# Kernel optimization log

Measured on AMD Instinct MI355X. Metric: run time of the kernel, lower is better.

## Reference

```python
import jax, jax.numpy as jnp
import numpy as np

NUM_CLASSES = 19
RMI_RADIUS = 3
POOL_SIZE = 3
POOL_STRIDE = 3
IGNORE_INDEX = 255
LOSS_WEIGHT = 1.0


def _avg_pool_nchw(x, k, s):
    # torch F.avg_pool2d with padding=k//2, count_include_pad=True
    p = k // 2
    summed = jax.lax.reduce_window(
        x, 0.0, jax.lax.add,
        window_dimensions=(1, 1, k, k),
        window_strides=(1, 1, s, s),
        padding=[(0, 0), (0, 0), (p, p), (p, p)])
    return summed / float(k * k)


def _map_get_pairs(labels, probs, radius):
    h, w = labels.shape[2], labels.shape[3]
    nh, nw = h - radius + 1, w - radius + 1
    la = jnp.stack([labels[:, :, y:y + nh, x:x + nw]
                    for y in range(radius) for x in range(radius)], axis=2)
    pr = jnp.stack([probs[:, :, y:y + nh, x:x + nw]
                    for y in range(radius) for x in range(radius)], axis=2)
    return la, pr  # (N, C, r*r, nh, nw)


def _log_det_by_cholesky(mat):
    chol = jnp.linalg.cholesky(mat)
    diag = jnp.diagonal(chol, axis1=-2, axis2=-1)
    return 2.0 * jnp.sum(jnp.log(diag + 1e-8), axis=-1)


def _rmi_lower_bound(labels_4d, probs_4d):
    labels_4d = _avg_pool_nchw(labels_4d, POOL_SIZE, POOL_STRIDE)
    probs_4d = _avg_pool_nchw(probs_4d, POOL_SIZE, POOL_STRIDE)
    la, pr = _map_get_pairs(labels_4d, probs_4d, RMI_RADIUS)
    N, C, D = la.shape[:3]
    la = la.reshape(N, C, D, -1)   # (N, C, D, M)
    pr = pr.reshape(N, C, D, -1)
    M = la.shape[-1]
    la = la - la.mean(axis=-1, keepdims=True)
    pr = pr - pr.mean(axis=-1, keepdims=True)
    la_cov = jnp.einsum('ncdm,ncem->ncde', la, la) / M
    pr_cov = jnp.einsum('ncdm,ncem->ncde', pr, pr) / M
    pr_la_cov = jnp.einsum('ncdm,ncem->ncde', pr, la) / M
    eye = jnp.eye(D, dtype=la_cov.dtype)
    la_cov_inv = jnp.linalg.inv(la_cov + eye * 1e-5)
    appro_var = pr_cov - jnp.einsum('ncde,ncef,ncgf->ncdg',
                                    pr_la_cov, la_cov_inv, pr_la_cov)
    appro_var = appro_var + eye * 1e-6
    rmi_per_class = 0.5 * _log_det_by_cholesky(appro_var)  # (N, C)
    rmi_per_class = rmi_per_class.mean(axis=0)             # (C,)
    return jnp.sum(rmi_per_class) / NUM_CLASSES


def setup_inputs() -> dict:
    key = jax.random.key(0)
    k1, k2 = jax.random.split(key)
    cls_score = jax.random.normal(k1, (4, 19, 512, 512), dtype=jnp.float32)
    label = jax.random.randint(k2, (4, 512, 512), 0, NUM_CLASSES, dtype=jnp.int64)
    return {"cls_score": cls_score, "label": label}


def reference(cls_score, label):
    probs = jax.nn.softmax(cls_score.astype(jnp.float32), axis=1)
    valid = (label >= 0) & (label < NUM_CLASSES) & (label != IGNORE_INDEX)
    lbl = jnp.where(valid, label, 0)
    onehot = jax.nn.one_hot(lbl, NUM_CLASSES, dtype=jnp.float32)
    onehot = jnp.transpose(onehot, (0, 3, 1, 2))  # (N, C, H, W)
    vmask = valid[:, None, :, :].astype(jnp.float32)
    onehot = onehot * vmask
    probs = probs * vmask
    loss = _rmi_lower_bound(onehot, probs)
    return LOSS_WEIGHT * loss
```

## Files before the change

### kernel.cpp

```cpp
#include <hip/hip_runtime.h>
#include <math.h>

#define NBATCH 4
#define NCLS   19
#define HWDIM  512
#define HW     (512 * 512)
#define PH     171
#define PHP    176
#define PP2A   (171 * 176)
#define NHW    169
#define MM     (169 * 169)

typedef float f4  __attribute__((ext_vector_type(4)));
typedef float f2v __attribute__((ext_vector_type(2)));

__global__ __launch_bounds__(512) void stage1_pool(
    const float* __restrict__ cls, const int* __restrict__ label,
    float* __restrict__ P, float* __restrict__ L) {
  int n  = blockIdx.x / PH;
  int ph = blockIdx.x - n * PH;
  int col = threadIdx.x;

  float vv[3][NCLS];
  int lbs[3];
#pragma unroll
  for (int i = 0; i < 3; ++i) {
    int r = 3 * ph - 1 + i;
    bool ok = (r >= 0) && (r < HWDIM);
    if (ok) {
      lbs[i] = label[((size_t)n * HWDIM + r) * HWDIM + col];
      const float* base = cls + (size_t)n * NCLS * HW + (size_t)r * HWDIM + col;
#pragma unroll
      for (int c = 0; c < NCLS; ++c) vv[i][c] = base[(size_t)c * HW];
    } else {
      lbs[i] = -1;
#pragma unroll
      for (int c = 0; c < NCLS; ++c) vv[i][c] = 0.f;
    }
  }

  float accP[NCLS], accL[NCLS];
#pragma unroll
  for (int c = 0; c < NCLS; ++c) { accP[c] = 0.f; accL[c] = 0.f; }
#pragma unroll
  for (int i = 0; i < 3; ++i) {
    int lb = lbs[i];
    float mx = vv[i][0];
#pragma unroll
    for (int c = 1; c < NCLS; ++c) mx = fmaxf(mx, vv[i][c]);
    float se = 0.f;
    float ex[NCLS];
#pragma unroll
    for (int c = 0; c < NCLS; ++c) {
      ex[c] = __expf(vv[i][c] - mx);
      se += ex[c];
    }
    float m = (lb >= 0 && lb < NCLS) ? 1.f : 0.f;
    float inv = m / se;
#pragma unroll
    for (int c = 0; c < NCLS; ++c) {
      accP[c] += ex[c] * inv;
      accL[c] += (lb == c) ? 1.f : 0.f;
    }
  }

  __shared__ float xbP[10][516];
  __shared__ float xbL[10][516];
  const float inv9 = 1.f / 9.f;
#pragma unroll
  for (int c0 = 0; c0 < NCLS; c0 += 10) {
#pragma unroll
    for (int cc = 0; cc < 10; ++cc) {
      if (c0 + cc < NCLS) {
        xbP[cc][1 + col] = accP[(c0 + cc) < NCLS ? (c0 + cc) : 0];
        xbL[cc][1 + col] = accL[(c0 + cc) < NCLS ? (c0 + cc) : 0];
        if (col == 0) { xbP[cc][0] = 0.f; xbL[cc][0] = 0.f; }
      }
    }
    __syncthreads();
    if (col < PH) {
      int pw = col;
#pragma unroll
      for (int cc = 0; cc < 10; ++cc) {
        if (c0 + cc < NCLS) {
          int c = c0 + cc;
          float sP = xbP[cc][3 * pw] + xbP[cc][3 * pw + 1] + xbP[cc][3 * pw + 2];
          float sL = xbL[cc][3 * pw] + xbL[cc][3 * pw + 1] + xbL[cc][3 * pw + 2];
          size_t o = ((size_t)(n * NCLS + c)) * PP2A + (size_t)ph * PHP + pw;
          P[o] = sP * inv9;
          L[o] = sL * inv9;
        }
      }
    } else if (col < PHP) {
#pragma unroll
      for (int cc = 0; cc < 10; ++cc) {
        if (c0 + cc < NCLS) {
          int c = c0 + cc;
          size_t o = ((size_t)(n * NCLS + c)) * PP2A + (size_t)ph * PHP + col;
          P[o] = 0.f;
          L[o] = 0.f;
        }
      }
    }
    __syncthreads();
  }
}

template <int MODE, int NA>
__device__ __forceinline__ void epilogue(const f2v (&acc2)[NA], float* red,
                                         float* __restrict__ covp, int nc) {
  int lane = threadIdx.x & 63;
  int wid  = threadIdx.x >> 6;
#pragma unroll
  for (int k = 0; k < NA; ++k) {
    float v = acc2[k].x + acc2[k].y;
    v += __shfl_down(v, 32, 64);
    v += __shfl_down(v, 16, 64);
    v += __shfl_down(v, 8, 64);
    if (lane < 8) red[(wid * 8 + lane) * 84 + k] = v;
  }
  __syncthreads();
  int tid = threadIdx.x;
  if (tid < NA) {
    float sm = 0.f;
#pragma unroll
    for (int w = 0; w < 64; ++w) sm += red[w * 84 + tid];
    int off;
    if (MODE == 0)      off = (tid < 9) ? tid : 18 + (tid - 9);
    else if (MODE == 1) off = (tid < 9) ? 9 + tid : 63 + (tid - 9);
    else                off = 108 + tid;
    covp[(size_t)nc * 192 + off] = sm;
  }
}

__device__ __forceinline__ void fma_self_triple(f2v (&acc2)[54],
    const f2v (&r0)[5], const f2v (&r1)[5], const f2v (&r2)[5]) {
#define RP(d, off) ((d) < 3 ? r0[(d) % 3 + (off)] \
                 : (d) < 6 ? r1[(d) % 3 + (off)] : r2[(d) % 3 + (off)])
#pragma unroll
  for (int d = 0; d < 9; ++d) {
    acc2[d] += RP(d, 0);
    acc2[d] += RP(d, 2);
  }
  {
    int k = 9;
#pragma unroll
    for (int d = 0; d < 9; ++d)
#pragma unroll
      for (int e = d; e < 9; ++e) {
        acc2[k] += RP(d, 0) * RP(e, 0);
        acc2[k] += RP(d, 2) * RP(e, 2);
        ++k;
      }
  }
#undef RP
}

__device__ __forceinline__ void fma_cross_triple(f2v (&acc2)[81],
    const f2v (&p0)[3], const f2v (&p1)[3], const f2v (&p2)[3],
    const f2v (&l0)[3], const f2v (&l1)[3], const f2v (&l2)[3]) {
#define QP(d) ((d) < 3 ? p0[(d) % 3] : (d) < 6 ? p1[(d) % 3] : p2[(d) % 3])
#define QL(e) ((e) < 3 ? l0[(e) % 3] : (e) < 6 ? l1[(e) % 3] : l2[(e) % 3])
#pragma unroll
  for (int d = 0; d < 9; ++d)
#pragma unroll
    for (int e = 0; e < 9; ++e)
      acc2[d * 9 + e] += QP(d) * QL(e);
#undef QP
#undef QL
}

template <int MODE>
__device__ __forceinline__ void mom_self(const float* __restrict__ X,
                                         float* __restrict__ covp, int nc,
                                         float* red) {
  f2v acc2[54];
#pragma unroll
  for (int k = 0; k < 54; ++k) acc2[k] = (f2v){0.f, 0.f};

  int tid = threadIdx.x;
  if (tid < 462) {
    int b = tid / 42, s = tid - b * 42;
    int x0 = 4 * s;
    int y0 = (NHW * b) / 11;
    int y1 = (NHW * (b + 1)) / 11;

    f2v s0[5], s1[5], s2[5], s3[5];
    auto ldr = [&](f2v (&dst)[5], int row) {
      if (row > PH - 1) row = PH - 1;
      f4  a  = *(const f4*)(X + row * PHP + x0);
      f2v bb = *(const f2v*)(X + row * PHP + x0 + 4);
      dst[0] = (f2v){a.x, a.y}; dst[1] = (f2v){a.y, a.z};
      dst[2] = (f2v){a.z, a.w}; dst[3] = (f2v){a.w, bb.x};
      dst[4] = bb;
    };
    ldr(s0, y0); ldr(s1, y0 + 1); ldr(s2, y0 + 2);

    int y = y0;
    int span = y1 - y0;
    int nf = span & ~3;
    for (int i = 0; i < nf; i += 4, y += 4) {
      ldr(s3, y + 3); fma_self_triple(acc2, s0, s1, s2);
      ldr(s0, y + 4); fma_self_triple(acc2, s1, s2, s3);
      ldr(s1, y + 5); fma_self_triple(acc2, s2, s3, s0);
      ldr(s2, y + 6); fma_self_triple(acc2, s3, s0, s1);
    }
    int r = span & 3;
    if (r > 0) { ldr(s3, y + 3); fma_self_triple(acc2, s0, s1, s2); ++y; }
    if (r > 1) { ldr(s0, y + 3); fma_self_triple(acc2, s1, s2, s3); ++y; }
    if (r > 2) { ldr(s1, y + 3); fma_self_triple(acc2, s2, s3, s0); ++y; }
  } else if (tid < 473) {
    int b  = tid - 462;
    int y0 = (NHW * b) / 11;
    int y1 = (NHW * (b + 1)) / 11;
    float t[3][3];
#pragma unroll
    for (int r = 0; r < 3; ++r)
#pragma unroll
      for (int c = 0; c < 3; ++c) t[r][c] = X[(y0 + r) * PHP + 168 + c];
    for (int y = y0; y < y1; ++y) {
      int yn = (y + 3 <= PH - 1) ? (y + 3) : (PH - 1);
      float n0 = X[yn * PHP + 168], n1 = X[yn * PHP + 169],
            n2 = X[yn * PHP + 170];
#pragma unroll
      for (int d = 0; d < 9; ++d) acc2[d].x += t[d / 3][d % 3];
      {
        int k = 9;
#pragma unroll
        for (int d = 0; d < 9; ++d)
#pragma unroll
          for (int e = d; e < 9; ++e) {
            acc2[k].x += t[d / 3][d % 3] * t[e / 3][e % 3];
            ++k;
          }
      }
#pragma unroll
      for (int c = 0; c < 3; ++c) { t[0][c] = t[1][c]; t[1][c] = t[2][c]; }
      t[2][0] = n0; t[2][1] = n1; t[2][2] = n2;
    }
  }
  epilogue<MODE, 54>(acc2, red, covp, nc);
}

__device__ __forceinline__ void mom_cross(const float* __restrict__ Pp,
                                          const float* __restrict__ Lp,
                                          float* __restrict__ covp, int nc,
                                          float* red) {
  f2v acc2[81];
#pragma unroll
  for (int k = 0; k < 81; ++k) acc2[k] = (f2v){0.f, 0.f};

  int tid = threadIdx.x;
  if (tid < 504) {
    int b = tid / 84, s = tid - b * 84;
    int x0 = 2 * s;
    int y0 = (NHW * b) / 6;
    int y1 = (NHW * (b + 1)) / 6;

    f2v p0[3], p1[3], p2[3], p3[3];
    f2v l0[3], l1[3], l2[3], l3[3];
    auto ldc = [&](f2v (&dp)[3], f2v (&dl)[3], int row) {
      if (row > PH - 1) row = PH - 1;
      f2v a = *(const f2v*)(Pp + row * PHP + x0);
      f2v bb = *(const f2v*)(Pp + row * PHP + x0 + 2);
      dp[0] = a; dp[1] = (f2v){a.y, bb.x}; dp[2] = bb;
      f2v c = *(const f2v*)(Lp + row * PHP + x0);
      f2v d = *(const f2v*)(Lp + row * PHP + x0 + 2);
      dl[0] = c; dl[1] = (f2v){c.y, d.x}; dl[2] = d;
    };
    ldc(p0, l0, y0); ldc(p1, l1, y0 + 1); ldc(p2, l2, y0 + 2);

    int y = y0;
    int span = y1 - y0;
    int nf = span & ~3;
    for (int i = 0; i < nf; i += 4, y += 4) {
      ldc(p3, l3, y + 3); fma_cross_triple(acc2, p0, p1, p2, l0, l1, l2);
      ldc(p0, l0, y + 4); fma_cross_triple(acc2, p1, p2, p3, l1, l2, l3);
      ldc(p1, l1, y + 5); fma_cross_triple(acc2, p2, p3, p0, l2, l3, l0);
      ldc(p2, l2, y + 6); fma_cross_triple(acc2, p3, p0, p1, l3, l0, l1);
    }
    int r = span & 3;
    if (r > 0) { ldc(p3, l3, y + 3); fma_cross_triple(acc2, p0, p1, p2, l0, l1, l2); ++y; }
    if (r > 1) { ldc(p0, l0, y + 3); fma_cross_triple(acc2, p1, p2, p3, l1, l2, l3); ++y; }
    if (r > 2) { ldc(p1, l1, y + 3); fma_cross_triple(acc2, p2, p3, p0, l2, l3, l0); ++y; }
  } else if (tid < 510) {
    int b  = tid - 504;
    int y0 = (NHW * b) / 6;
    int y1 = (NHW * (b + 1)) / 6;
    float tp[3][3], tl[3][3];
#pragma unroll
    for (int r = 0; r < 3; ++r)
#pragma unroll
      for (int c = 0; c < 3; ++c) {
        tp[r][c] = Pp[(y0 + r) * PHP + 168 + c];
        tl[r][c] = Lp[(y0 + r) * PHP + 168 + c];
      }
    for (int y = y0; y < y1; ++y) {
      int yn = (y + 3 <= PH - 1) ? (y + 3) : (PH - 1);
      float np0 = Pp[yn * PHP + 168], np1 = Pp[yn * PHP + 169],
            np2 = Pp[yn * PHP + 170];
      float nl0 = Lp[yn * PHP + 168], nl1 = Lp[yn * PHP + 169],
            nl2 = Lp[yn * PHP + 170];
#pragma unroll
      for (int d = 0; d < 9; ++d)
#pragma unroll
        for (int e = 0; e < 9; ++e)
          acc2[d * 9 + e].x += tp[d / 3][d % 3] * tl[e / 3][e % 3];
#pragma unroll
      for (int c = 0; c < 3; ++c) {
        tp[0][c] = tp[1][c]; tp[1][c] = tp[2][c];
        tl[0][c] = tl[1][c]; tl[1][c] = tl[2][c];
      }
      tp[2][0] = np0; tp[2][1] = np1; tp[2][2] = np2;
      tl[2][0] = nl0; tl[2][1] = nl1; tl[2][2] = nl2;
    }
  }
  epilogue<2, 81>(acc2, red, covp, nc);
}

__global__ __launch_bounds__(512) void stage2_mom(
    const float* __restrict__ P, const float* __restrict__ L,
    float* __restrict__ covp) {
  __shared__ float red[64 * 84];
  int nc = blockIdx.x;
  const float* Pp = P + (size_t)nc * PP2A;
  const float* Lp = L + (size_t)nc * PP2A;
  if (blockIdx.y == 0)      mom_self<0>(Lp, covp, nc, red);
  else if (blockIdx.y == 1) mom_self<1>(Pp, covp, nc, red);
  else                      mom_cross(Pp, Lp, covp, nc, red);
}

__global__ __launch_bounds__(64) void stage3_rmi(float* __restrict__ covp) {
  int nc  = blockIdx.x;
  int tid = threadIdx.x;
  const float* s = covp + (size_t)nc * 192;
  __shared__ double lc[81], pc[81], plc[81], mla[9], mpr[9];
  const double Minv = 1.0 / (double)MM;

  if (tid < 9)       mla[tid]     = (double)s[tid] * Minv;
  else if (tid < 18) mpr[tid - 9] = (double)s[tid] * Minv;
  __syncthreads();

  for (int e = tid; e < 81; e += 64) {
    int r = e / 9, c = e - 9 * (e / 9);
    int lo = r < c ? r : c, hi = r < c ? c : r;
    int k = lo * 9 - lo * (lo - 1) / 2 + (hi - lo);
    double a = (double)s[18 + k] * Minv - mla[r] * mla[c];
    if (r == c) a += 1e-5;
    lc[e] = a;
    pc[e] = (double)s[63 + k] * Minv - mpr[r] * mpr[c];
    plc[e] = (double)s[108 + e] * Minv - mpr[r] * mla[c];
  }
  __syncthreads();

  for (int j = 0; j < 9; ++j) {
    if (tid == 0) lc[j * 9 + j] = sqrt(lc[j * 9 + j]);
    __syncthreads();
    if (tid > j && tid < 9) lc[tid * 9 + j] /= lc[j * 9 + j];
    __syncthreads();
    if (tid > j && tid < 9) {
      double lij = lc[tid * 9 + j];
      for (int k = j + 1; k <= tid; ++k) lc[tid * 9 + k] -= lij * lc[k * 9 + j];
    }
    __syncthreads();
  }

  if (tid < 9) {
    int d = tid;
    for (int j = 0; j < 9; ++j) {
      double t = plc[d * 9 + j];
      for (int k = 0; k < j; ++k) t -= plc[d * 9 + k] * lc[j * 9 + k];
      plc[d * 9 + j] = t / lc[j * 9 + j];
    }
  }
  __syncthreads();

  for (int e = tid; e < 81; e += 64) {
    int r = e / 9, c = e - 9 * (e / 9);
    double a = pc[e];
    for (int f = 0; f < 9; ++f) a -= plc[r * 9 + f] * plc[c * 9 + f];
    if (r == c) a += 1e-6;
    pc[e] = a;
  }
  __syncthreads();

  for (int j = 0; j < 9; ++j) {
    if (tid == 0) pc[j * 9 + j] = sqrt(pc[j * 9 + j]);
    __syncthreads();
    if (tid > j && tid < 9) pc[tid * 9 + j] /= pc[j * 9 + j];
    __syncthreads();
    if (tid > j && tid < 9) {
      double lij = pc[tid * 9 + j];
      for (int k = j + 1; k <= tid; ++k) pc[tid * 9 + k] -= lij * pc[k * 9 + j];
    }
    __syncthreads();
  }

  if (tid == 0) {
    double sl = 0.0;
    for (int j = 0; j < 9; ++j) sl += log(pc[j * 9 + j] + 1e-8);
    *(double*)(covp + (size_t)nc * 192 + 190) = sl;
  }
}

__global__ __launch_bounds__(64) void stage4_reduce(
    const float* __restrict__ covp, float* __restrict__ out) {
  int tid = threadIdx.x;
  double v = 0.0;
  if (tid < NBATCH * NCLS)
    v = *(const double*)(covp + (size_t)tid * 192 + 190);
  if (tid + 64 < NBATCH * NCLS)
    v += *(const double*)(covp + (size_t)(tid + 64) * 192 + 190);
#pragma unroll
  for (int o = 32; o > 0; o >>= 1) v += __shfl_down(v, o, 64);
  if (tid == 0) out[0] = (float)(v / (double)(NBATCH * NCLS));
}

extern "C" void kernel_launch(void* const* d_in, const int* in_sizes, int n_in,
                              void* d_out, int out_size, void* d_ws, size_t ws_size,
                              hipStream_t stream) {
  const float* cls  = (const float*)d_in[0];
  const int* label  = (const int*)d_in[1];
  float* out = (float*)d_out;

  float* P    = (float*)d_ws;
  float* L    = P + (size_t)NBATCH * NCLS * PP2A;
  float* covp = L + (size_t)NBATCH * NCLS * PP2A;

  stage1_pool<<<NBATCH * PH, 512, 0, stream>>>(cls, label, P, L);
  dim3 g2(NBATCH * NCLS, 3, 1);
  stage2_mom<<<g2, 512, 0, stream>>>(P, L, covp);
  stage3_rmi<<<NBATCH * NCLS, 64, 0, stream>>>(covp);
  stage4_reduce<<<1, 64, 0, stream>>>(covp, out);
}
```

Baseline: 72.49 us.

## Split cross-covariance moment block into three row-offset blocks

The 81-entry cross-covariance accumulation is split across three separate blocks, one per probability row offset G, so each block holds 27 accumulators instead of 81. This lowers register pressure in the heaviest block and raises the stage-2 grid from 3 to 5 blocks per (n,c), evening out the load across blocks. In exchange, the label rows are reloaded in each of the three blocks and the launch has more blocks.

```diff
diff --git a/kernel.cpp b/kernel.cpp
--- a/kernel.cpp
+++ b/kernel.cpp
@@ -128,7 +128,7 @@
     int off;
     if (MODE == 0)      off = (tid < 9) ? tid : 18 + (tid - 9);
     else if (MODE == 1) off = (tid < 9) ? 9 + tid : 63 + (tid - 9);
-    else                off = 108 + tid;
+    else                off = 108 + 27 * (MODE - 2) + tid;
     covp[(size_t)nc * 192 + off] = sm;
   }
 }
@@ -156,17 +156,15 @@
 #undef RP
 }
 
-__device__ __forceinline__ void fma_cross_triple(f2v (&acc2)[81],
-    const f2v (&p0)[3], const f2v (&p1)[3], const f2v (&p2)[3],
+__device__ __forceinline__ void fma_cross_g(f2v (&acc2)[27],
+    const f2v (&q)[3],
     const f2v (&l0)[3], const f2v (&l1)[3], const f2v (&l2)[3]) {
-#define QP(d) ((d) < 3 ? p0[(d) % 3] : (d) < 6 ? p1[(d) % 3] : p2[(d) % 3])
 #define QL(e) ((e) < 3 ? l0[(e) % 3] : (e) < 6 ? l1[(e) % 3] : l2[(e) % 3])
 #pragma unroll
-  for (int d = 0; d < 9; ++d)
+  for (int dx = 0; dx < 3; ++dx)
 #pragma unroll
     for (int e = 0; e < 9; ++e)
-      acc2[d * 9 + e] += QP(d) * QL(e);
-#undef QP
+      acc2[dx * 9 + e] += q[dx] * QL(e);
 #undef QL
 }
 
@@ -242,13 +240,14 @@
   epilogue<MODE, 54>(acc2, red, covp, nc);
 }
 
-__device__ __forceinline__ void mom_cross(const float* __restrict__ Pp,
-                                          const float* __restrict__ Lp,
-                                          float* __restrict__ covp, int nc,
-                                          float* red) {
-  f2v acc2[81];
-#pragma unroll
-  for (int k = 0; k < 81; ++k) acc2[k] = (f2v){0.f, 0.f};
+template <int G>
+__device__ __forceinline__ void mom_cross_g(const float* __restrict__ Pp,
+                                            const float* __restrict__ Lp,
+                                            float* __restrict__ covp, int nc,
+                                            float* red) {
+  f2v acc2[27];
+#pragma unroll
+  for (int k = 0; k < 27; ++k) acc2[k] = (f2v){0.f, 0.f};
 
   int tid = threadIdx.x;
   if (tid < 504) {
@@ -257,65 +256,58 @@
     int y0 = (NHW * b) / 6;
     int y1 = (NHW * (b + 1)) / 6;
 
-    f2v p0[3], p1[3], p2[3], p3[3];
     f2v l0[3], l1[3], l2[3], l3[3];
-    auto ldc = [&](f2v (&dp)[3], f2v (&dl)[3], int row) {
+    f2v q0[3], q1[3];
+    auto ldl = [&](f2v (&d)[3], int row) {
       if (row > PH - 1) row = PH - 1;
-      f2v a = *(const f2v*)(Pp + row * PHP + x0);
+      f2v a  = *(const f2v*)(Lp + row * PHP + x0);
+      f2v bb = *(const f2v*)(Lp + row * PHP + x0 + 2);
+      d[0] = a; d[1] = (f2v){a.y, bb.x}; d[2] = bb;
+    };
+    auto ldq = [&](f2v (&d)[3], int row) {
+      if (row > PH - 1) row = PH - 1;
+      f2v a  = *(const f2v*)(Pp + row * PHP + x0);
       f2v bb = *(const f2v*)(Pp + row * PHP + x0 + 2);
-      dp[0] = a; dp[1] = (f2v){a.y, bb.x}; dp[2] = bb;
-      f2v c = *(const f2v*)(Lp + row * PHP + x0);
-      f2v d = *(const f2v*)(Lp + row * PHP + x0 + 2);
-      dl[0] = c; dl[1] = (f2v){c.y, d.x}; dl[2] = d;
+      d[0] = a; d[1] = (f2v){a.y, bb.x}; d[2] = bb;
     };
-    ldc(p0, l0, y0); ldc(p1, l1, y0 + 1); ldc(p2, l2, y0 + 2);
+    ldl(l0, y0); ldl(l1, y0 + 1); ldl(l2, y0 + 2); ldq(q0, y0 + G);
 
     int y = y0;
     int span = y1 - y0;
     int nf = span & ~3;
     for (int i = 0; i < nf; i += 4, y += 4) {
-      ldc(p3, l3, y + 3); fma_cross_triple(acc2, p0, p1, p2, l0, l1, l2);
-      ldc(p0, l0, y + 4); fma_cross_triple(acc2, p1, p2, p3, l1, l2, l3);
-      ldc(p1, l1, y + 5); fma_cross_triple(acc2, p2, p3, p0, l2, l3, l0);
-      ldc(p2, l2, y + 6); fma_cross_triple(acc2, p3, p0, p1, l3, l0, l1);
+      ldl(l3, y + 3); ldq(q1, y + G + 1); fma_cross_g(acc2, q0, l0, l1, l2);
+      ldl(l0, y + 4); ldq(q0, y + G + 2); fma_cross_g(acc2, q1, l1, l2, l3);
+      ldl(l1, y + 5); ldq(q1, y + G + 3); fma_cross_g(acc2, q0, l2, l3, l0);
+      ldl(l2, y + 6); ldq(q0, y + G + 4); fma_cross_g(acc2, q1, l3, l0, l1);
     }
     int r = span & 3;
-    if (r > 0) { ldc(p3, l3, y + 3); fma_cross_triple(acc2, p0, p1, p2, l0, l1, l2); ++y; }
-    if (r > 1) { ldc(p0, l0, y + 3); fma_cross_triple(acc2, p1, p2, p3, l1, l2, l3); ++y; }
-    if (r > 2) { ldc(p1, l1, y + 3); fma_cross_triple(acc2, p2, p3, p0, l2, l3, l0); ++y; }
+    if (r > 0) { ldl(l3, y + 3); ldq(q1, y + G + 1);
+                 fma_cross_g(acc2, q0, l0, l1, l2); ++y; }
+    if (r > 1) { ldl(l0, y + 3); ldq(q0, y + G + 2);
+                 fma_cross_g(acc2, q1, l1, l2, l3); ++y; }
+    if (r > 2) { ldl(l1, y + 3); ldq(q1, y + G + 3);
+                 fma_cross_g(acc2, q0, l2, l3, l0); ++y; }
   } else if (tid < 510) {
     int b  = tid - 504;
     int y0 = (NHW * b) / 6;
     int y1 = (NHW * (b + 1)) / 6;
-    float tp[3][3], tl[3][3];
-#pragma unroll
-    for (int r = 0; r < 3; ++r)
+    for (int y = y0; y < y1; ++y) {
+      float q[3], t[3][3];
 #pragma unroll
       for (int c = 0; c < 3; ++c) {
-        tp[r][c] = Pp[(y0 + r) * PHP + 168 + c];
-        tl[r][c] = Lp[(y0 + r) * PHP + 168 + c];
-      }
-    for (int y = y0; y < y1; ++y) {
-      int yn = (y + 3 <= PH - 1) ? (y + 3) : (PH - 1);
-      float np0 = Pp[yn * PHP + 168], np1 = Pp[yn * PHP + 169],
-            np2 = Pp[yn * PHP + 170];
-      float nl0 = Lp[yn * PHP + 168], nl1 = Lp[yn * PHP + 169],
-            nl2 = Lp[yn * PHP + 170];
-#pragma unroll
-      for (int d = 0; d < 9; ++d)
+        q[c] = Pp[(y + G) * PHP + 168 + c];
+#pragma unroll
+        for (int rr = 0; rr < 3; ++rr) t[rr][c] = Lp[(y + rr) * PHP + 168 + c];
+      }
+#pragma unroll
+      for (int dx = 0; dx < 3; ++dx)
 #pragma unroll
         for (int e = 0; e < 9; ++e)
-          acc2[d * 9 + e].x += tp[d / 3][d % 3] * tl[e / 3][e % 3];
-#pragma unroll
-      for (int c = 0; c < 3; ++c) {
-        tp[0][c] = tp[1][c]; tp[1][c] = tp[2][c];
-        tl[0][c] = tl[1][c]; tl[1][c] = tl[2][c];
-      }
-      tp[2][0] = np0; tp[2][1] = np1; tp[2][2] = np2;
-      tl[2][0] = nl0; tl[2][1] = nl1; tl[2][2] = nl2;
-    }
-  }
-  epilogue<2, 81>(acc2, red, covp, nc);
+          acc2[dx * 9 + e].x += q[dx] * t[e / 3][e % 3];
+    }
+  }
+  epilogue<2 + G, 27>(acc2, red, covp, nc);
 }
 
 __global__ __launch_bounds__(512) void stage2_mom(
@@ -325,9 +317,13 @@
   int nc = blockIdx.x;
   const float* Pp = P + (size_t)nc * PP2A;
   const float* Lp = L + (size_t)nc * PP2A;
-  if (blockIdx.y == 0)      mom_self<0>(Lp, covp, nc, red);
-  else if (blockIdx.y == 1) mom_self<1>(Pp, covp, nc, red);
-  else                      mom_cross(Pp, Lp, covp, nc, red);
+  switch (blockIdx.y) {
+    case 0: mom_self<0>(Lp, covp, nc, red); break;
+    case 1: mom_self<1>(Pp, covp, nc, red); break;
+    case 2: mom_cross_g<0>(Pp, Lp, covp, nc, red); break;
+    case 3: mom_cross_g<1>(Pp, Lp, covp, nc, red); break;
+    default: mom_cross_g<2>(Pp, Lp, covp, nc, red); break;
+  }
 }
 
 __global__ __launch_bounds__(64) void stage3_rmi(float* __restrict__ covp) {
@@ -428,7 +424,7 @@
   float* covp = L + (size_t)NBATCH * NCLS * PP2A;
 
   stage1_pool<<<NBATCH * PH, 512, 0, stream>>>(cls, label, P, L);
-  dim3 g2(NBATCH * NCLS, 3, 1);
+  dim3 g2(NBATCH * NCLS, 5, 1);
   stage2_mom<<<g2, 512, 0, stream>>>(P, L, covp);
   stage3_rmi<<<NBATCH * NCLS, 64, 0, stream>>>(covp);
   stage4_reduce<<<1, 64, 0, stream>>>(covp, out);
```

Measured after the change: 78.13 us. +7.8%, slower.

## Stage pooled rows through LDS in chunks for moment accumulation

Applied to the files above, without the earlier changes.

Stage 2 no longer streams sliding row windows from global memory per thread. Each block now cooperatively copies chunks of about 30 rows into shared memory (up to 2x32x176 floats), synchronises, then every thread reads its three-row windows from LDS. The aim is to replace redundant uncoalesced global loads with coalesced bulk copies and LDS reads. In exchange it adds barriers per chunk, drops the register-level row rotation so each row is re-read three times from LDS, and raises LDS use to about 45KB, which may lower occupancy.

```diff
diff --git a/kernel.cpp b/kernel.cpp
--- a/kernel.cpp
+++ b/kernel.cpp
@@ -10,6 +10,8 @@
 #define PP2A   (171 * 176)
 #define NHW    169
 #define MM     (169 * 169)
+#define NCHUNK 6
+#define LROWS  32
 
 typedef float f4  __attribute__((ext_vector_type(4)));
 typedef float f2v __attribute__((ext_vector_type(2)));
@@ -109,6 +111,7 @@
 template <int MODE, int NA>
 __device__ __forceinline__ void epilogue(const f2v (&acc2)[NA], float* red,
                                          float* __restrict__ covp, int nc) {
+  __syncthreads();
   int lane = threadIdx.x & 63;
   int wid  = threadIdx.x >> 6;
 #pragma unroll
@@ -173,161 +176,158 @@
 template <int MODE>
 __device__ __forceinline__ void mom_self(const float* __restrict__ X,
                                          float* __restrict__ covp, int nc,
-                                         float* red) {
+                                         float* sbuf) {
   f2v acc2[54];
 #pragma unroll
   for (int k = 0; k < 54; ++k) acc2[k] = (f2v){0.f, 0.f};
 
   int tid = threadIdx.x;
-  if (tid < 462) {
-    int b = tid / 42, s = tid - b * 42;
-    int x0 = 4 * s;
-    int y0 = (NHW * b) / 11;
-    int y1 = (NHW * (b + 1)) / 11;
-
-    f2v s0[5], s1[5], s2[5], s3[5];
-    auto ldr = [&](f2v (&dst)[5], int row) {
-      if (row > PH - 1) row = PH - 1;
-      f4  a  = *(const f4*)(X + row * PHP + x0);
-      f2v bb = *(const f2v*)(X + row * PHP + x0 + 4);
-      dst[0] = (f2v){a.x, a.y}; dst[1] = (f2v){a.y, a.z};
-      dst[2] = (f2v){a.z, a.w}; dst[3] = (f2v){a.w, bb.x};
-      dst[4] = bb;
-    };
-    ldr(s0, y0); ldr(s1, y0 + 1); ldr(s2, y0 + 2);
-
-    int y = y0;
-    int span = y1 - y0;
-    int nf = span & ~3;
-    for (int i = 0; i < nf; i += 4, y += 4) {
-      ldr(s3, y + 3); fma_self_triple(acc2, s0, s1, s2);
-      ldr(s0, y + 4); fma_self_triple(acc2, s1, s2, s3);
-      ldr(s1, y + 5); fma_self_triple(acc2, s2, s3, s0);
-      ldr(s2, y + 6); fma_self_triple(acc2, s3, s0, s1);
-    }
-    int r = span & 3;
-    if (r > 0) { ldr(s3, y + 3); fma_self_triple(acc2, s0, s1, s2); ++y; }
-    if (r > 1) { ldr(s0, y + 3); fma_self_triple(acc2, s1, s2, s3); ++y; }
-    if (r > 2) { ldr(s1, y + 3); fma_self_triple(acc2, s2, s3, s0); ++y; }
-  } else if (tid < 473) {
-    int b  = tid - 462;
-    int y0 = (NHW * b) / 11;
-    int y1 = (NHW * (b + 1)) / 11;
-    float t[3][3];
-#pragma unroll
-    for (int r = 0; r < 3; ++r)
-#pragma unroll
-      for (int c = 0; c < 3; ++c) t[r][c] = X[(y0 + r) * PHP + 168 + c];
-    for (int y = y0; y < y1; ++y) {
-      int yn = (y + 3 <= PH - 1) ? (y + 3) : (PH - 1);
-      float n0 = X[yn * PHP + 168], n1 = X[yn * PHP + 169],
-            n2 = X[yn * PHP + 170];
-#pragma unroll
-      for (int d = 0; d < 9; ++d) acc2[d].x += t[d / 3][d % 3];
-      {
-        int k = 9;
-#pragma unroll
-        for (int d = 0; d < 9; ++d)
-#pragma unroll
-          for (int e = d; e < 9; ++e) {
-            acc2[k].x += t[d / 3][d % 3] * t[e / 3][e % 3];
-            ++k;
-          }
-      }
-#pragma unroll
-      for (int c = 0; c < 3; ++c) { t[0][c] = t[1][c]; t[1][c] = t[2][c]; }
-      t[2][0] = n0; t[2][1] = n1; t[2][2] = n2;
-    }
-  }
-  epilogue<MODE, 54>(acc2, red, covp, nc);
+  bool full = (tid < 462);
+  bool tail = (tid >= 462 && tid < 473);
+  int s  = full ? (tid - (tid / 42) * 42) : 0;
+  int b  = full ? (tid / 42) : (tid - 462);
+  int x0 = 4 * s;
+
+  for (int k = 0; k < NCHUNK; ++k) {
+    int w0 = (NHW * k) / NCHUNK;
+    int w1 = (NHW * (k + 1)) / NCHUNK;
+    int span = w1 - w0;
+    int nf4 = (span + 2) * 44;
+    __syncthreads();
+    {
+      const float* src = X + w0 * PHP;
+      for (int i = tid; i < nf4; i += 512)
+        *(f4*)&sbuf[4 * i] = *(const f4*)(src + 4 * i);
+    }
+    __syncthreads();
+
+    if (full) {
+      int ys = (span * b) / 11, ye = (span * (b + 1)) / 11;
+      for (int r = ys; r < ye; ++r) {
+        f2v wa[5], wb[5], wc[5];
+#pragma unroll
+        for (int rr = 0; rr < 3; ++rr) {
+          const float* p = sbuf + (r + rr) * PHP + x0;
+          f2v a = *(const f2v*)p;
+          f2v m = *(const f2v*)(p + 2);
+          f2v c = *(const f2v*)(p + 4);
+          f2v* w = (rr == 0) ? wa : (rr == 1) ? wb : wc;
+          w[0] = a; w[1] = (f2v){a.y, m.x}; w[2] = m;
+          w[3] = (f2v){m.y, c.x}; w[4] = c;
+        }
+        fma_self_triple(acc2, wa, wb, wc);
+      }
+    } else if (tail) {
+      int ys = (span * b) / 11, ye = (span * (b + 1)) / 11;
+      for (int r = ys; r < ye; ++r) {
+        float t[3][3];
+#pragma unroll
+        for (int rr = 0; rr < 3; ++rr)
+#pragma unroll
+          for (int cc = 0; cc < 3; ++cc)
+            t[rr][cc] = sbuf[(r + rr) * PHP + 168 + cc];
+#pragma unroll
+        for (int d = 0; d < 9; ++d) acc2[d].x += t[d / 3][d % 3];
+        {
+          int kk = 9;
+#pragma unroll
+          for (int d = 0; d < 9; ++d)
+#pragma unroll
+            for (int e = d; e < 9; ++e) {
+              acc2[kk].x += t[d / 3][d % 3] * t[e / 3][e % 3];
+              ++kk;
+            }
+        }
+      }
+    }
+  }
+  epilogue<MODE, 54>(acc2, sbuf, covp, nc);
 }
 
 __device__ __forceinline__ void mom_cross(const float* __restrict__ Pp,
                                           const float* __restrict__ Lp,
                                           float* __restrict__ covp, int nc,
-                                          float* red) {
+                                          float* sbuf) {
   f2v acc2[81];
 #pragma unroll
   for (int k = 0; k < 81; ++k) acc2[k] = (f2v){0.f, 0.f};
 
+  float* sP = sbuf;
+  float* sL = sbuf + LROWS * PHP;
   int tid = threadIdx.x;
-  if (tid < 504) {
-    int b = tid / 84, s = tid - b * 84;
-    int x0 = 2 * s;
-    int y0 = (NHW * b) / 6;
-    int y1 = (NHW * (b + 1)) / 6;
-
-    f2v p0[3], p1[3], p2[3], p3[3];
-    f2v l0[3], l1[3], l2[3], l3[3];
-    auto ldc = [&](f2v (&dp)[3], f2v (&dl)[3], int row) {
-      if (row > PH - 1) row = PH - 1;
-      f2v a = *(const f2v*)(Pp + row * PHP + x0);
-      f2v bb = *(const f2v*)(Pp + row * PHP + x0 + 2);
-      dp[0] = a; dp[1] = (f2v){a.y, bb.x}; dp[2] = bb;
-      f2v c = *(const f2v*)(Lp + row * PHP + x0);
-      f2v d = *(const f2v*)(Lp + row * PHP + x0 + 2);
-      dl[0] = c; dl[1] = (f2v){c.y, d.x}; dl[2] = d;
-    };
-    ldc(p0, l0, y0); ldc(p1, l1, y0 + 1); ldc(p2, l2, y0 + 2);
-
-    int y = y0;
-    int span = y1 - y0;
-    int nf = span & ~3;
-    for (int i = 0; i < nf; i += 4, y += 4) {
-      ldc(p3, l3, y + 3); fma_cross_triple(acc2, p0, p1, p2, l0, l1, l2);
-      ldc(p0, l0, y + 4); fma_cross_triple(acc2, p1, p2, p3, l1, l2, l3);
-      ldc(p1, l1, y + 5); fma_cross_triple(acc2, p2, p3, p0, l2, l3, l0);
-      ldc(p2, l2, y + 6); fma_cross_triple(acc2, p3, p0, p1, l3, l0, l1);
-    }
-    int r = span & 3;
-    if (r > 0) { ldc(p3, l3, y + 3); fma_cross_triple(acc2, p0, p1, p2, l0, l1, l2); ++y; }
-    if (r > 1) { ldc(p0, l0, y + 3); fma_cross_triple(acc2, p1, p2, p3, l1, l2, l3); ++y; }
-    if (r > 2) { ldc(p1, l1, y + 3); fma_cross_triple(acc2, p2, p3, p0, l2, l3, l0); ++y; }
-  } else if (tid < 510) {
-    int b  = tid - 504;
-    int y0 = (NHW * b) / 6;
-    int y1 = (NHW * (b + 1)) / 6;
-    float tp[3][3], tl[3][3];
-#pragma unroll
-    for (int r = 0; r < 3; ++r)
-#pragma unroll
-      for (int c = 0; c < 3; ++c) {
-        tp[r][c] = Pp[(y0 + r) * PHP + 168 + c];
-        tl[r][c] = Lp[(y0 + r) * PHP + 168 + c];
-      }
-    for (int y = y0; y < y1; ++y) {
-      int yn = (y + 3 <= PH - 1) ? (y + 3) : (PH - 1);
-      float np0 = Pp[yn * PHP + 168], np1 = Pp[yn * PHP + 169],
-            np2 = Pp[yn * PHP + 170];
-      float nl0 = Lp[yn * PHP + 168], nl1 = Lp[yn * PHP + 169],
-            nl2 = Lp[yn * PHP + 170];
-#pragma unroll
-      for (int d = 0; d < 9; ++d)
-#pragma unroll
-        for (int e = 0; e < 9; ++e)
-          acc2[d * 9 + e].x += tp[d / 3][d % 3] * tl[e / 3][e % 3];
-#pragma unroll
-      for (int c = 0; c < 3; ++c) {
-        tp[0][c] = tp[1][c]; tp[1][c] = tp[2][c];
-        tl[0][c] = tl[1][c]; tl[1][c] = tl[2][c];
-      }
-      tp[2][0] = np0; tp[2][1] = np1; tp[2][2] = np2;
-      tl[2][0] = nl0; tl[2][1] = nl1; tl[2][2] = nl2;
-    }
-  }
-  epilogue<2, 81>(acc2, red, covp, nc);
+  bool full = (tid < 504);
+  bool tail = (tid >= 504 && tid < 510);
+  int s  = full ? (tid - (tid / 84) * 84) : 0;
+  int b  = full ? (tid / 84) : (tid - 504);
+  int x0 = 2 * s;
+
+  for (int k = 0; k < NCHUNK; ++k) {
+    int w0 = (NHW * k) / NCHUNK;
+    int w1 = (NHW * (k + 1)) / NCHUNK;
+    int span = w1 - w0;
+    int nf4 = (span + 2) * 44;
+    __syncthreads();
+    {
+      const float* srcP = Pp + w0 * PHP;
+      const float* srcL = Lp + w0 * PHP;
+      for (int i = tid; i < nf4; i += 512) {
+        *(f4*)&sP[4 * i] = *(const f4*)(srcP + 4 * i);
+        *(f4*)&sL[4 * i] = *(const f4*)(srcL + 4 * i);
+      }
+    }
+    __syncthreads();
+
+    if (full) {
+      int ys = (span * b) / 6, ye = (span * (b + 1)) / 6;
+      for (int r = ys; r < ye; ++r) {
+        f2v p0[3], p1[3], p2[3], l0[3], l1[3], l2[3];
+#pragma unroll
+        for (int rr = 0; rr < 3; ++rr) {
+          const float* pp = sP + (r + rr) * PHP + x0;
+          f2v a = *(const f2v*)pp;
+          f2v c = *(const f2v*)(pp + 2);
+          f2v* w = (rr == 0) ? p0 : (rr == 1) ? p1 : p2;
+          w[0] = a; w[1] = (f2v){a.y, c.x}; w[2] = c;
+          const float* pl = sL + (r + rr) * PHP + x0;
+          f2v al = *(const f2v*)pl;
+          f2v cl = *(const f2v*)(pl + 2);
+          f2v* wl = (rr == 0) ? l0 : (rr == 1) ? l1 : l2;
+          wl[0] = al; wl[1] = (f2v){al.y, cl.x}; wl[2] = cl;
+        }
+        fma_cross_triple(acc2, p0, p1, p2, l0, l1, l2);
+      }
+    } else if (tail) {
+      int ys = (span * b) / 6, ye = (span * (b + 1)) / 6;
+      for (int r = ys; r < ye; ++r) {
+        float tp[3][3], tl[3][3];
+#pragma unroll
+        for (int rr = 0; rr < 3; ++rr)
+#pragma unroll
+          for (int cc = 0; cc < 3; ++cc) {
+            tp[rr][cc] = sP[(r + rr) * PHP + 168 + cc];
+            tl[rr][cc] = sL[(r + rr) * PHP + 168 + cc];
+          }
+#pragma unroll
+        for (int d = 0; d < 9; ++d)
+#pragma unroll
+          for (int e = 0; e < 9; ++e)
+            acc2[d * 9 + e].x += tp[d / 3][d % 3] * tl[e / 3][e % 3];
+      }
+    }
+  }
+  epilogue<2, 81>(acc2, sbuf, covp, nc);
 }
 
 __global__ __launch_bounds__(512) void stage2_mom(
     const float* __restrict__ P, const float* __restrict__ L,
     float* __restrict__ covp) {
-  __shared__ float red[64 * 84];
+  __shared__ float sbuf[2 * LROWS * PHP];
   int nc = blockIdx.x;
   const float* Pp = P + (size_t)nc * PP2A;
   const float* Lp = L + (size_t)nc * PP2A;
-  if (blockIdx.y == 0)      mom_self<0>(Lp, covp, nc, red);
-  else if (blockIdx.y == 1) mom_self<1>(Pp, covp, nc, red);
-  else                      mom_cross(Pp, Lp, covp, nc, red);
+  if (blockIdx.y == 0)      mom_self<0>(Lp, covp, nc, sbuf);
+  else if (blockIdx.y == 1) mom_self<1>(Pp, covp, nc, sbuf);
+  else                      mom_cross(Pp, Lp, covp, nc, sbuf);
 }
 
 __global__ __launch_bounds__(64) void stage3_rmi(float* __restrict__ covp) {
```

After: 77.68 us. 7.2% more time.

## Vectorize stage1 pooling loads with float4 per thread across three rows

Applied to the files above, without the earlier changes.

Stage1 now maps 384 threads onto 3 rows times 128 float4 column groups, so each thread loads four pixels per class with a 128-bit load and computes the softmax for one row only, instead of one column across three rows. Horizontal and vertical 3x3 summation moves into shared memory, which is staged in chunks of 4 classes. The aim is wider memory transactions and lower register pressure in this bandwidth-bound pass. The cost is more barriers (5 class chunks instead of 2) and shared-memory reads for the vertical reduction.

```diff
diff --git a/kernel.cpp b/kernel.cpp
--- a/kernel.cpp
+++ b/kernel.cpp
@@ -14,89 +14,101 @@
 typedef float f4  __attribute__((ext_vector_type(4)));
 typedef float f2v __attribute__((ext_vector_type(2)));
 
-__global__ __launch_bounds__(512) void stage1_pool(
+__global__ __launch_bounds__(384) void stage1_pool(
     const float* __restrict__ cls, const int* __restrict__ label,
     float* __restrict__ P, float* __restrict__ L) {
-  int n  = blockIdx.x / PH;
-  int ph = blockIdx.x - n * PH;
-  int col = threadIdx.x;
-
-  float vv[3][NCLS];
-  int lbs[3];
-#pragma unroll
-  for (int i = 0; i < 3; ++i) {
-    int r = 3 * ph - 1 + i;
-    bool ok = (r >= 0) && (r < HWDIM);
-    if (ok) {
-      lbs[i] = label[((size_t)n * HWDIM + r) * HWDIM + col];
-      const float* base = cls + (size_t)n * NCLS * HW + (size_t)r * HWDIM + col;
-#pragma unroll
-      for (int c = 0; c < NCLS; ++c) vv[i][c] = base[(size_t)c * HW];
-    } else {
-      lbs[i] = -1;
-#pragma unroll
-      for (int c = 0; c < NCLS; ++c) vv[i][c] = 0.f;
-    }
-  }
-
-  float accP[NCLS], accL[NCLS];
-#pragma unroll
-  for (int c = 0; c < NCLS; ++c) { accP[c] = 0.f; accL[c] = 0.f; }
-#pragma unroll
-  for (int i = 0; i < 3; ++i) {
-    int lb = lbs[i];
-    float mx = vv[i][0];
-#pragma unroll
-    for (int c = 1; c < NCLS; ++c) mx = fmaxf(mx, vv[i][c]);
-    float se = 0.f;
-    float ex[NCLS];
+  int n   = blockIdx.x / PH;
+  int ph  = blockIdx.x - n * PH;
+  int t   = threadIdx.x;
+  int row = t >> 7;
+  int c4  = (t & 127) << 2;
+
+  int r = 3 * ph - 1 + row;
+  bool rowok = (r >= 0) && (r < HWDIM);
+
+  f4 v[NCLS];
+  f4 inv4 = (f4){0.f, 0.f, 0.f, 0.f};
+  int lb0 = -1, lb1 = -1, lb2 = -1, lb3 = -1;
+
+  if (rowok) {
+    const int4 lq = *(const int4*)(label + ((size_t)n * HWDIM + r) * HWDIM + c4);
+    lb0 = lq.x; lb1 = lq.y; lb2 = lq.z; lb3 = lq.w;
+    const float* base = cls + (size_t)n * NCLS * HW + (size_t)r * HWDIM + c4;
+#pragma unroll
+    for (int c = 0; c < NCLS; ++c)
+      v[c] = *(const f4*)(base + (size_t)c * HW);
+
+    f4 mx = v[0];
+#pragma unroll
+    for (int c = 1; c < NCLS; ++c) {
+#pragma unroll
+      for (int j = 0; j < 4; ++j) mx[j] = fmaxf(mx[j], v[c][j]);
+    }
+    f4 se = (f4){0.f, 0.f, 0.f, 0.f};
 #pragma unroll
     for (int c = 0; c < NCLS; ++c) {
-      ex[c] = __expf(vv[i][c] - mx);
-      se += ex[c];
-    }
-    float m = (lb >= 0 && lb < NCLS) ? 1.f : 0.f;
-    float inv = m / se;
-#pragma unroll
-    for (int c = 0; c < NCLS; ++c) {
-      accP[c] += ex[c] * inv;
-      accL[c] += (lb == c) ? 1.f : 0.f;
-    }
-  }
-
-  __shared__ float xbP[10][516];
-  __shared__ float xbL[10][516];
+#pragma unroll
+      for (int j = 0; j < 4; ++j) {
+        v[c][j] = __expf(v[c][j] - mx[j]);
+        se[j] += v[c][j];
+      }
+    }
+    inv4.x = (lb0 >= 0 && lb0 < NCLS) ? 1.f / se.x : 0.f;
+    inv4.y = (lb1 >= 0 && lb1 < NCLS) ? 1.f / se.y : 0.f;
+    inv4.z = (lb2 >= 0 && lb2 < NCLS) ? 1.f / se.z : 0.f;
+    inv4.w = (lb3 >= 0 && lb3 < NCLS) ? 1.f / se.w : 0.f;
+  } else {
+#pragma unroll
+    for (int c = 0; c < NCLS; ++c) v[c] = (f4){0.f, 0.f, 0.f, 0.f};
+  }
+
+  __shared__ float xbP[3][4][512];
+  __shared__ float xbL[3][4][512];
   const float inv9 = 1.f / 9.f;
-#pragma unroll
-  for (int c0 = 0; c0 < NCLS; c0 += 10) {
-#pragma unroll
-    for (int cc = 0; cc < 10; ++cc) {
-      if (c0 + cc < NCLS) {
-        xbP[cc][1 + col] = accP[(c0 + cc) < NCLS ? (c0 + cc) : 0];
-        xbL[cc][1 + col] = accL[(c0 + cc) < NCLS ? (c0 + cc) : 0];
-        if (col == 0) { xbP[cc][0] = 0.f; xbL[cc][0] = 0.f; }
-      }
-    }
-    __syncthreads();
-    if (col < PH) {
-      int pw = col;
-#pragma unroll
-      for (int cc = 0; cc < 10; ++cc) {
-        if (c0 + cc < NCLS) {
-          int c = c0 + cc;
-          float sP = xbP[cc][3 * pw] + xbP[cc][3 * pw + 1] + xbP[cc][3 * pw + 2];
-          float sL = xbL[cc][3 * pw] + xbL[cc][3 * pw + 1] + xbL[cc][3 * pw + 2];
-          size_t o = ((size_t)(n * NCLS + c)) * PP2A + (size_t)ph * PHP + pw;
+
+#pragma unroll
+  for (int c0 = 0; c0 < NCLS; c0 += 4) {
+#pragma unroll
+    for (int cc = 0; cc < 4; ++cc) {
+      int c = c0 + cc;
+      if (c < NCLS) {
+        f4 pv, lv;
+#pragma unroll
+        for (int j = 0; j < 4; ++j) pv[j] = v[c][j] * inv4[j];
+        lv.x = (lb0 == c) ? 1.f : 0.f;
+        lv.y = (lb1 == c) ? 1.f : 0.f;
+        lv.z = (lb2 == c) ? 1.f : 0.f;
+        lv.w = (lb3 == c) ? 1.f : 0.f;
+        *(f4*)&xbP[row][cc][c4] = pv;
+        *(f4*)&xbL[row][cc][c4] = lv;
+      }
+    }
+    __syncthreads();
+    if (t < PH) {
+      int x0 = 3 * t - 1;
+      int xi = (x0 < 0) ? 0 : x0;
+      float g = (t > 0) ? 1.f : 0.f;
+#pragma unroll
+      for (int cc = 0; cc < 4; ++cc) {
+        int c = c0 + cc;
+        if (c < NCLS) {
+          float sP = 0.f, sL = 0.f;
+#pragma unroll
+          for (int i = 0; i < 3; ++i) {
+            sP += xbP[i][cc][xi] * g + xbP[i][cc][x0 + 1] + xbP[i][cc][x0 + 2];
+            sL += xbL[i][cc][xi] * g + xbL[i][cc][x0 + 1] + xbL[i][cc][x0 + 2];
+          }
+          size_t o = ((size_t)(n * NCLS + c)) * PP2A + (size_t)ph * PHP + t;
           P[o] = sP * inv9;
           L[o] = sL * inv9;
         }
       }
-    } else if (col < PHP) {
-#pragma unroll
-      for (int cc = 0; cc < 10; ++cc) {
-        if (c0 + cc < NCLS) {
-          int c = c0 + cc;
-          size_t o = ((size_t)(n * NCLS + c)) * PP2A + (size_t)ph * PHP + col;
+    } else if (t < PHP) {
+#pragma unroll
+      for (int cc = 0; cc < 4; ++cc) {
+        int c = c0 + cc;
+        if (c < NCLS) {
+          size_t o = ((size_t)(n * NCLS + c)) * PP2A + (size_t)ph * PHP + t;
           P[o] = 0.f;
           L[o] = 0.f;
         }
@@ -427,7 +439,7 @@
   float* L    = P + (size_t)NBATCH * NCLS * PP2A;
   float* covp = L + (size_t)NBATCH * NCLS * PP2A;
 
-  stage1_pool<<<NBATCH * PH, 512, 0, stream>>>(cls, label, P, L);
+  stage1_pool<<<NBATCH * PH, 384, 0, stream>>>(cls, label, P, L);
   dim3 g2(NBATCH * NCLS, 3, 1);
   stage2_mom<<<g2, 512, 0, stream>>>(P, L, covp);
   stage3_rmi<<<NBATCH * NCLS, 64, 0, stream>>>(covp);
```

New measurement: 77.28 us. +6.6%, slower.
